# Performance work log

Measured on AMD Instinct MI355X. Metric: run time of the kernel, lower is better.

Reference implementation:

```python
import jax, jax.numpy as jnp
import numpy as np

V, D, NH, HD, FF, NL, NLOOPS = 1056, 320, 5, 64, 864, 6, 8
CAP, EPS, THETA = 0.8, 1e-6, 10000.0
B, S = 8, 2048


def rmsnorm(x, w):
    return w * (x * jax.lax.rsqrt(jnp.mean(x * x, axis=-1, keepdims=True) + EPS))


def rotate_half(x):
    x1, x2 = jnp.split(x, 2, axis=-1)
    return jnp.concatenate([-x2, x1], axis=-1)


def rope_tables(seq_len):
    freqs = 1.0 / (THETA ** (jnp.arange(0, HD, 2, dtype=jnp.float32) / HD))  # [HD/2]
    t = jnp.arange(seq_len, dtype=jnp.float32)
    f = jnp.outer(t, freqs)                      # [S, HD/2]
    f = jnp.concatenate([f, f], axis=-1)         # [S, HD]
    return jnp.cos(f), jnp.sin(f)


def setup_inputs() -> dict:
    key = jax.random.key(0)
    ks = jax.random.split(key, 12)
    std = 0.02
    inp = {
        "input_ids": jax.random.randint(ks[0], (B, S), 0, V),
        "iteration": 0,
        "embedding": jax.random.normal(ks[1], (V, D), jnp.float32),
        "iter_emb": jax.random.normal(ks[2], (NLOOPS, D), jnp.float32),
        "attn_norm_w": jnp.ones((NL, D), jnp.float32),
        "Wqkv": jax.random.normal(ks[3], (NL, 3 * D, D), jnp.float32) * std,
        "wo_w": jax.random.normal(ks[4], (NL, D, D), jnp.float32) * std,
        "router_w": jax.random.normal(ks[5], (NL, D), jnp.float32) * std,
        "mlp_norm_w": jnp.ones((NL, D), jnp.float32),
        "gate_w": jax.random.normal(ks[6], (NL, FF, D), jnp.float32) * std,
        "up_w": jax.random.normal(ks[7], (NL, FF, D), jnp.float32) * std,
        "down_w": jax.random.normal(ks[8], (NL, D, FF), jnp.float32) * std,
        "final_norm_w": jnp.ones((D,), jnp.float32),
    }
    return inp


def reference(input_ids, iteration, embedding, iter_emb, attn_norm_w, Wqkv, wo_w,
              router_w, mlp_norm_w, gate_w, up_w, down_w, final_norm_w):
    batch, seq = input_ids.shape
    k = max(1, int(seq * CAP))
    cos, sin = rope_tables(seq)                 # [S, HD]
    cos4 = cos[None, :, None, :]                # [1,S,1,HD]
    sin4 = sin[None, :, None, :]

    x = embedding[input_ids]                    # [B,S,D]
    if iteration < NLOOPS:
        x = x + iter_emb[iteration][None, None, :]

    causal = jnp.tril(jnp.ones((seq, seq), dtype=bool))
    bidx = jnp.arange(batch)[:, None]           # [B,1]

    for l in range(NL):
        # --- attention block ---
        h = rmsnorm(x, attn_norm_w[l])
        qkv = (h @ Wqkv[l].T).reshape(batch, seq, 3, NH, HD)
        q, kk, v = qkv[:, :, 0], qkv[:, :, 1], qkv[:, :, 2]   # [B,S,H,HD]
        q = q * cos4 + rotate_half(q) * sin4
        kk = kk * cos4 + rotate_half(kk) * sin4
        q, kk, v = (t.transpose(0, 2, 1, 3) for t in (q, kk, v))  # [B,H,S,HD]
        scores = jnp.einsum("bhqd,bhkd->bhqk", q, kk) / np.sqrt(HD)
        scores = jnp.where(causal, scores, -jnp.inf)
        attn = jax.nn.softmax(scores, axis=-1)
        out = jnp.einsum("bhqk,bhkd->bhqd", attn, v)
        out = out.transpose(0, 2, 1, 3).reshape(batch, seq, D)
        x = x + out @ wo_w[l].T

        # --- MoD router + SwiGLU MLP on selected tokens ---
        probs = jax.nn.sigmoid(x @ router_w[l])            # [B,S]
        topk_probs, topk_idx = jax.lax.top_k(probs, k)     # [B,K]
        sel = jnp.take_along_axis(x, topk_idx[:, :, None], axis=1)  # [B,K,D]
        hs = rmsnorm(sel, mlp_norm_w[l])
        gate = jax.nn.silu(hs @ gate_w[l].T) * (hs @ up_w[l].T)
        mlp = (gate @ down_w[l].T) * topk_probs[:, :, None]         # [B,K,D]
        x = x.at[bidx, topk_idx].add(mlp)                  # unique idx: add == scatter-set+residual

    return rmsnorm(x, final_norm_w)
```

## Files before the change

### kernel.cpp

```cpp
#include <hip/hip_runtime.h>
#include <hip/hip_bf16.h>
#include <math.h>

#define VSZ 1056
#define DD 320
#define NH 5
#define HD 64
#define FF 864
#define NL 6
#define NLOOPS 8
#define BB 8
#define SL 2048
#define KK 1638
#define EPSF 1e-6f

typedef _Float16 f16x8 __attribute__((ext_vector_type(8)));
typedef _Float16 f16x4 __attribute__((ext_vector_type(4)));
typedef float floatx16 __attribute__((ext_vector_type(16)));

__device__ inline void gll16(const void* g, void* l) {
    __builtin_amdgcn_global_load_lds((const __attribute__((address_space(1))) void*)g,
                                     (__attribute__((address_space(3))) void*)l, 16, 0, 0);
}

__global__ __launch_bounds__(256) void cast4_kernel(const float* __restrict__ s,
        _Float16* __restrict__ d, int n4) {
    int i = blockIdx.x * 256 + threadIdx.x;
    if (i >= n4) return;
    float4 v = ((const float4*)s)[i];
    f16x4 o = { (_Float16)v.x, (_Float16)v.y, (_Float16)v.z, (_Float16)v.w };
    *(f16x4*)(d + (size_t)i * 4) = o;
}

__global__ __launch_bounds__(256) void embed_kernel(const int* __restrict__ ids,
        const int* __restrict__ iter, const float* __restrict__ emb,
        const float* __restrict__ iter_emb, float* __restrict__ x) {
    int i = blockIdx.x * 256 + threadIdx.x;
    int d = i % DD, bs = i / DD;
    float v = emb[(size_t)ids[bs] * DD + d];
    int it = iter[0];
    if (it < NLOOPS) v += iter_emb[it * DD + d];
    x[i] = v;
}

template<typename OT>
__global__ __launch_bounds__(256) void rmsnorm_kernel(const float* __restrict__ x,
        const float* __restrict__ w, OT* __restrict__ out, int nrows) {
    int row = blockIdx.x * 4 + (threadIdx.x >> 6);
    int lane = threadIdx.x & 63;
    if (row >= nrows) return;
    const float* xr = x + (size_t)row * DD;
    float v[5]; float ss = 0.f;
#pragma unroll
    for (int i = 0; i < 5; ++i) { v[i] = xr[lane + i * 64]; ss += v[i] * v[i]; }
#pragma unroll
    for (int o = 32; o > 0; o >>= 1) ss += __shfl_xor(ss, o);
    float r = rsqrtf(ss * (1.f / DD) + EPSF);
    OT* orow = out + (size_t)row * DD;
#pragma unroll
    for (int i = 0; i < 5; ++i) orow[lane + i * 64] = (OT)(w[lane + i * 64] * v[i] * r);
}

__global__ __launch_bounds__(256) void gather_rmsnorm_kernel(const float* __restrict__ x,
        const int* __restrict__ tkidx, const float* __restrict__ w,
        _Float16* __restrict__ out, int nrows) {
    int row = blockIdx.x * 4 + (threadIdx.x >> 6);
    int lane = threadIdx.x & 63;
    if (row >= nrows) return;
    int b = row / KK;
    int t = tkidx[row];
    const float* xr = x + ((size_t)b * SL + t) * DD;
    float v[5]; float ss = 0.f;
#pragma unroll
    for (int i = 0; i < 5; ++i) { v[i] = xr[lane + i * 64]; ss += v[i] * v[i]; }
#pragma unroll
    for (int o = 32; o > 0; o >>= 1) ss += __shfl_xor(ss, o);
    float r = rsqrtf(ss * (1.f / DD) + EPSF);
    _Float16* orow = out + (size_t)row * DD;
#pragma unroll
    for (int i = 0; i < 5; ++i) orow[lane + i * 64] = (_Float16)(w[lane + i * 64] * v[i] * r);
}

__global__ __launch_bounds__(256) void router_kernel(const float* __restrict__ x,
        const float* __restrict__ rw, float* __restrict__ probs, int nrows) {
    int row = blockIdx.x * 4 + (threadIdx.x >> 6);
    int lane = threadIdx.x & 63;
    if (row >= nrows) return;
    const float* xr = x + (size_t)row * DD;
    float ss = 0.f;
#pragma unroll
    for (int i = 0; i < 5; ++i) ss += xr[lane + i * 64] * rw[lane + i * 64];
#pragma unroll
    for (int o = 32; o > 0; o >>= 1) ss += __shfl_xor(ss, o);
    if (lane == 0) probs[row] = 1.f / (1.f + __expf(-ss));
}

__global__ __launch_bounds__(1024) void topk_kernel(const float* __restrict__ probs,
        int* __restrict__ tkidx, float* __restrict__ tkprob) {
    __shared__ int hist[256];
    __shared__ int scn[256];
    __shared__ int outc;
    __shared__ int s_digit, s_rem;
    int b = blockIdx.x, tid = threadIdx.x;
    unsigned long long k0, k1;
    {
        unsigned int f0 = __float_as_uint(probs[b * SL + tid]);
        unsigned int f1 = __float_as_uint(probs[b * SL + tid + 1024]);
        k0 = ((unsigned long long)f0 << 32) | (unsigned int)(2047 - tid);
        k1 = ((unsigned long long)f1 << 32) | (unsigned int)(2047 - (tid + 1024));
    }
    if (tid == 0) outc = 0;
    unsigned long long prefix = 0, pmask = 0;
    int target = KK;
    for (int shift = 56; shift >= 0; shift -= 8) {
        if (tid < 256) hist[tid] = 0;
        __syncthreads();
        bool a0 = (k0 & pmask) == prefix;
        bool a1 = (k1 & pmask) == prefix;
        int d0 = (int)((k0 >> shift) & 255);
        int d1 = (int)((k1 >> shift) & 255);
        if (a0) atomicAdd(&hist[d0], 1);
        if (a1) atomicAdd(&hist[d1], 1);
        __syncthreads();
        if (tid < 256) scn[tid] = hist[tid];
        __syncthreads();
#pragma unroll
        for (int st = 1; st < 256; st <<= 1) {
            int v = 0;
            if (tid < 256 && tid + st < 256) v = scn[tid + st];
            __syncthreads();
            if (tid < 256) scn[tid] += v;
            __syncthreads();
        }
        if (tid < 256 && hist[tid] > 0) {
            int S = scn[tid];
            int Sgt = S - hist[tid];
            if (Sgt < target && target <= S) { s_digit = tid; s_rem = target - Sgt; }
        }
        __syncthreads();
        int dsel = s_digit, rem = s_rem;
        bool full = (rem == hist[dsel]);
        if (a0 && (d0 > dsel || (full && d0 == dsel))) {
            int s = atomicAdd(&outc, 1);
            tkidx[b * KK + s] = 2047 - (int)(k0 & 0xffffffffu);
            tkprob[b * KK + s] = __uint_as_float((unsigned int)(k0 >> 32));
        }
        if (a1 && (d1 > dsel || (full && d1 == dsel))) {
            int s = atomicAdd(&outc, 1);
            tkidx[b * KK + s] = 2047 - (int)(k1 & 0xffffffffu);
            tkprob[b * KK + s] = __uint_as_float((unsigned int)(k1 >> 32));
        }
        if (full) break;
        target = rem;
        prefix |= ((unsigned long long)dsel) << shift;
        pmask  |= ((unsigned long long)255) << shift;
        __syncthreads();
    }
}

__global__ __launch_bounds__(256) void prep_kernel(const _Float16* __restrict__ qkv,
        _Float16* __restrict__ Qh, _Float16* __restrict__ Kt, _Float16* __restrict__ Vt) {
    __shared__ _Float16 vt[64][72];
    int tid = threadIdx.x;
    int t = blockIdx.x, h = blockIdx.y, b = blockIdx.z;
    int bh = b * NH + h;
    int c = tid >> 5;
    int slb = tid & 31;
    const float QS = 0.125f * 1.44269504088896341f;
#pragma unroll
    for (int half = 0; half < 2; ++half) {
        int sl = half * 32 + slb;
        int s = t * 64 + sl;
        size_t rbase = ((size_t)(b * SL + s) * 3) * (NH * 64) + h * 64;
        f16x8 qv = *(const f16x8*)(qkv + rbase + c * 8);
        f16x8 qp = *(const f16x8*)(qkv + rbase + (c ^ 4) * 8);
        f16x8 kv = *(const f16x8*)(qkv + rbase + NH * 64 + c * 8);
        f16x8 kp = *(const f16x8*)(qkv + rbase + NH * 64 + (c ^ 4) * 8);
        f16x8 vv = *(const f16x8*)(qkv + rbase + 2 * NH * 64 + c * 8);
        f16x8 qo, ko;
#pragma unroll
        for (int j = 0; j < 8; ++j) {
            int d = c * 8 + j;
            float freq = exp2f(-(float)(d & 31) * 0.4152410118609203f);
            float ang = (float)s * freq;
            float cc = cosf(ang), sn = sinf(ang);
            float a = (float)qv[j], p = (float)qp[j];
            float ka = (float)kv[j], kb2 = (float)kp[j];
            float qr = (d < 32) ? a * cc - p * sn : a * cc + p * sn;
            float kr = (d < 32) ? ka * cc - kb2 * sn : ka * cc + kb2 * sn;
            qo[j] = (_Float16)(qr * QS);
            ko[j] = (_Float16)kr;
        }
        *(f16x8*)(Qh + ((size_t)bh * SL + s) * 64 + c * 8) = qo;
        *(f16x8*)(Kt + (((size_t)bh * 32 + t) * 8 + c) * 512 + sl * 8) = ko;
        *(f16x8*)(&vt[sl][c * 8]) = vv;
    }
    __syncthreads();
#pragma unroll
    for (int gg = 0; gg < 2; ++gg) {
        int oo = tid * 16 + gg * 8;
        int kc = oo >> 9;
        int d = (oo >> 3) & 63;
        f16x8 vo;
#pragma unroll
        for (int j = 0; j < 8; ++j) vo[j] = vt[kc * 8 + j][d];
        *(f16x8*)(Vt + (((size_t)bh * 32 + t) * 8 + kc) * 512 + d * 8) = vo;
    }
}

__global__ __launch_bounds__(256, 2) void attn_mfma(const _Float16* __restrict__ Qh,
        const _Float16* __restrict__ Kt, const _Float16* __restrict__ Vt,
        _Float16* __restrict__ attn_out) {
    __shared__ float red[4][64][33];
    __shared__ float msh[4][32];
    __shared__ float lsh[4][32];
    int tid = threadIdx.x;
    int w = tid >> 6;
    int lane = tid & 63;
    int l31 = lane & 31, h5 = lane >> 5;
    int g = blockIdx.x;
    int j = g >> 3;
    int bh = (g & 7) + 8 * (j >> 6);
    int qt = 63 - (j & 63);
    int b = bh / NH, h = bh % NH;
    int nt = (qt >> 1) + 1;
    int qw = qt * 32;
    int myq = qw + l31;

    f16x8 qf[4];
    const _Float16* qrow = Qh + ((size_t)bh * SL + myq) * 64;
#pragma unroll
    for (int kd = 0; kd < 4; ++kd) qf[kd] = *(const f16x8*)(qrow + kd * 16 + h5 * 8);

    const _Float16* Kb = Kt + (size_t)bh * 32 * 4096;
    const _Float16* Vb = Vt + (size_t)bh * 32 * 4096;

    floatx16 O0, O1;
#pragma unroll
    for (int r = 0; r < 16; ++r) { O0[r] = 0.f; O1[r] = 0.f; }
    float m = -INFINITY, l = 0.f;

    for (int t = w; t < nt; t += 4) {
        const _Float16* kb = Kb + (size_t)t * 4096;
        const _Float16* vb = Vb + (size_t)t * 4096;
        f16x8 a0[4], a1[4], v0[4], v1[4];
#pragma unroll
        for (int kd = 0; kd < 4; ++kd) {
            int off = (kd * 2 + h5) * 512 + l31 * 8;
            a0[kd] = *(const f16x8*)(kb + off);
            a1[kd] = *(const f16x8*)(kb + off + 256);
        }
#pragma unroll
        for (int kc = 0; kc < 4; ++kc) {
            int off = (kc * 2 + h5) * 512 + l31 * 8;
            v0[kc] = *(const f16x8*)(vb + off);
            v1[kc] = *(const f16x8*)(vb + off + 256);
        }
        floatx16 S0, S1;
#pragma unroll
        for (int r = 0; r < 16; ++r) { S0[r] = 0.f; S1[r] = 0.f; }
#pragma unroll
        for (int kd = 0; kd < 4; ++kd) {
            S0 = __builtin_amdgcn_mfma_f32_32x32x16_f16(a0[kd], qf[kd], S0, 0, 0, 0);
            S1 = __builtin_amdgcn_mfma_f32_32x32x16_f16(a1[kd], qf[kd], S1, 0, 0, 0);
        }
        int t0 = t * 64;
        if (t0 + 63 > qw) {
#pragma unroll
            for (int r = 0; r < 16; ++r) {
                int key = t0 + (r & 3) + 8 * (r >> 2) + 4 * h5;
                if (key > myq) S0[r] = -INFINITY;
                if (key + 32 > myq) S1[r] = -INFINITY;
            }
        }
        float tmax = S0[0];
#pragma unroll
        for (int r = 1; r < 16; ++r) tmax = fmaxf(tmax, S0[r]);
#pragma unroll
        for (int r = 0; r < 16; ++r) tmax = fmaxf(tmax, S1[r]);
        tmax = fmaxf(tmax, __shfl_xor(tmax, 32));
        if (__any(tmax > m + 8.f)) {
            float mnew = fmaxf(m, tmax);
            float alpha = exp2f(m - mnew);
            l *= alpha; O0 *= alpha; O1 *= alpha; m = mnew;
        }
        float P0[16], P1[16]; float psum = 0.f;
#pragma unroll
        for (int r = 0; r < 16; ++r) { P0[r] = exp2f(S0[r] - m); psum += P0[r]; }
#pragma unroll
        for (int r = 0; r < 16; ++r) { P1[r] = exp2f(S1[r] - m); psum += P1[r]; }
        psum += __shfl_xor(psum, 32);
        l += psum;
#pragma unroll
        for (int sub = 0; sub < 2; ++sub) {
            const float* P = sub ? P1 : P0;
#pragma unroll
            for (int kk = 0; kk < 2; ++kk) {
                float lo[4], hi[4], plo[4], phi[4];
#pragma unroll
                for (int k = 0; k < 4; ++k) { lo[k] = P[kk * 8 + k]; hi[k] = P[kk * 8 + 4 + k]; }
#pragma unroll
                for (int k = 0; k < 4; ++k) { plo[k] = __shfl_xor(lo[k], 32); phi[k] = __shfl_xor(hi[k], 32); }
                f16x8 pf;
#pragma unroll
                for (int k = 0; k < 4; ++k) {
                    pf[k]     = (_Float16)(h5 ? phi[k] : lo[k]);
                    pf[4 + k] = (_Float16)(h5 ? hi[k] : plo[k]);
                }
                int ksg = sub * 2 + kk;
                O0 = __builtin_amdgcn_mfma_f32_32x32x16_f16(v0[ksg], pf, O0, 0, 0, 0);
                O1 = __builtin_amdgcn_mfma_f32_32x32x16_f16(v1[ksg], pf, O1, 0, 0, 0);
            }
        }
    }
    if (h5 == 0) msh[w][l31] = m;
    __syncthreads();
    float M = fmaxf(fmaxf(msh[0][l31], msh[1][l31]), fmaxf(msh[2][l31], msh[3][l31]));
    float wgt = exp2f(m - M);
    if (h5 == 0) lsh[w][l31] = l * wgt;
#pragma unroll
    for (int r = 0; r < 16; ++r) {
        int d = (r & 3) + 8 * (r >> 2) + 4 * h5;
        red[w][d][l31] = O0[r] * wgt;
        red[w][d + 32][l31] = O1[r] * wgt;
    }
    __syncthreads();
    float lsum = lsh[0][l31] + lsh[1][l31] + lsh[2][l31] + lsh[3][l31];
    float linv = 1.f / lsum;
    f16x8 ov;
#pragma unroll
    for (int k = 0; k < 8; ++k) {
        int d = w * 16 + h5 * 8 + k;
        ov[k] = (_Float16)((red[0][d][l31] + red[1][d][l31] +
                            red[2][d][l31] + red[3][d][l31]) * linv);
    }
    *(f16x8*)(attn_out + ((size_t)(b * SL + myq)) * DD + h * 64 + w * 16 + h5 * 8) = ov;
}

template<int MODE>
__global__ __launch_bounds__(256) void gemm_mfma(const _Float16* __restrict__ A,
        const _Float16* __restrict__ W, _Float16* __restrict__ Ch, float* __restrict__ X,
        int M, int N, int K, const int* __restrict__ sidx, const float* __restrict__ sprob) {
    __shared__ __attribute__((aligned(16))) _Float16 As[4096];
    __shared__ __attribute__((aligned(16))) _Float16 Ws[4096];
    int tid = threadIdx.x;
    int lane = tid & 63;
    int wave = tid >> 6;
    int l31 = lane & 31, h5 = lane >> 5;
    int m0 = blockIdx.y * 128, n0 = blockIdx.x * 128;
    int wm = (wave & 1) * 64, wn = (wave >> 1) * 64;

    int srow = tid & 127;
    int skc = tid >> 7;
    int arow = m0 + srow; if (arow >= M) arow = M - 1;
    int wrow = n0 + srow; if (wrow >= N) wrow = N - 1;
    const _Float16* Ag = A + (size_t)arow * K + skc * 8;
    const _Float16* Wg = W + (size_t)wrow * K + skc * 8;
    _Float16* AsD = As + (size_t)(tid & ~63) * 8;
    _Float16* WsD = Ws + (size_t)(tid & ~63) * 8;

    floatx16 acc[2][2];
#pragma unroll
    for (int i = 0; i < 2; ++i)
#pragma unroll
        for (int j = 0; j < 2; ++j)
#pragma unroll
            for (int r = 0; r < 16; ++r) acc[i][j][r] = 0.f;

    for (int k0 = 0; k0 < K; k0 += 32) {
        __syncthreads();
        gll16(Ag + k0, AsD);
        gll16(Ag + k0 + 16, AsD + 2048);
        gll16(Wg + k0, WsD);
        gll16(Wg + k0 + 16, WsD + 2048);
        __syncthreads();
#pragma unroll
        for (int ks = 0; ks < 2; ++ks) {
            int kc = ks * 2 + h5;
            f16x8 a0 = *(const f16x8*)(As + kc * 1024 + (wm + l31) * 8);
            f16x8 a1 = *(const f16x8*)(As + kc * 1024 + (wm + 32 + l31) * 8);
            f16x8 b0 = *(const f16x8*)(Ws + kc * 1024 + (wn + l31) * 8);
            f16x8 b1 = *(const f16x8*)(Ws + kc * 1024 + (wn + 32 + l31) * 8);
            acc[0][0] = __builtin_amdgcn_mfma_f32_32x32x16_f16(a0, b0, acc[0][0], 0, 0, 0);
            acc[0][1] = __builtin_amdgcn_mfma_f32_32x32x16_f16(a0, b1, acc[0][1], 0, 0, 0);
            acc[1][0] = __builtin_amdgcn_mfma_f32_32x32x16_f16(a1, b0, acc[1][0], 0, 0, 0);
            acc[1][1] = __builtin_amdgcn_mfma_f32_32x32x16_f16(a1, b1, acc[1][1], 0, 0, 0);
        }
    }

#pragma unroll
    for (int ti = 0; ti < 2; ++ti) {
#pragma unroll
        for (int r = 0; r < 16; ++r) {
            int mm = m0 + wm + ti * 32 + (r & 3) + 8 * (r >> 2) + 4 * h5;
            if (mm >= M) continue;
            float scale = 1.f;
            float* xrow = nullptr;
            _Float16* crow = nullptr;
            if (MODE == 2) {
                int b = mm / KK;
                scale = sprob[mm];
                xrow = X + ((size_t)(b * SL + sidx[mm])) * N;
            } else if (MODE == 1) {
                xrow = X + (size_t)mm * N;
            } else {
                crow = Ch + (size_t)mm * N;
            }
#pragma unroll
            for (int tj = 0; tj < 2; ++tj) {
                int nn = n0 + wn + tj * 32 + l31;
                if (nn >= N) continue;
                float v = acc[ti][tj][r];
                if (MODE == 0) crow[nn] = (_Float16)v;
                else if (MODE == 1) xrow[nn] += v;
                else xrow[nn] += v * scale;
            }
        }
    }
}

__global__ __launch_bounds__(256) void gemm_gateup(const _Float16* __restrict__ A,
        const _Float16* __restrict__ Wg, const _Float16* __restrict__ Wu,
        _Float16* __restrict__ Ch, int M, int N, int K) {
    __shared__ __attribute__((aligned(16))) _Float16 As[4096];
    __shared__ __attribute__((aligned(16))) _Float16 Wgs[4096];
    __shared__ __attribute__((aligned(16))) _Float16 Wus[4096];
    int tid = threadIdx.x;
    int lane = tid & 63;
    int wave = tid >> 6;
    int l31 = lane & 31, h5 = lane >> 5;
    int m0 = blockIdx.y * 128, n0 = blockIdx.x * 128;
    int wm = (wave & 1) * 64, wn = (wave >> 1) * 64;

    int srow = tid & 127;
    int skc = tid >> 7;
    int arow = m0 + srow; if (arow >= M) arow = M - 1;
    int wrow = n0 + srow; if (wrow >= N) wrow = N - 1;
    const _Float16* Ag  = A  + (size_t)arow * K + skc * 8;
    const _Float16* Wgg = Wg + (size_t)wrow * K + skc * 8;
    const _Float16* Wug = Wu + (size_t)wrow * K + skc * 8;
    _Float16* AsD  = As  + (size_t)(tid & ~63) * 8;
    _Float16* WgsD = Wgs + (size_t)(tid & ~63) * 8;
    _Float16* WusD = Wus + (size_t)(tid & ~63) * 8;

    floatx16 ag[2][2], au[2][2];
#pragma unroll
    for (int i = 0; i < 2; ++i)
#pragma unroll
        for (int j = 0; j < 2; ++j)
#pragma unroll
            for (int r = 0; r < 16; ++r) { ag[i][j][r] = 0.f; au[i][j][r] = 0.f; }

    for (int k0 = 0; k0 < K; k0 += 32) {
        __syncthreads();
        gll16(Ag + k0, AsD);
        gll16(Ag + k0 + 16, AsD + 2048);
        gll16(Wgg + k0, WgsD);
        gll16(Wgg + k0 + 16, WgsD + 2048);
        gll16(Wug + k0, WusD);
        gll16(Wug + k0 + 16, WusD + 2048);
        __syncthreads();
#pragma unroll
        for (int ks = 0; ks < 2; ++ks) {
            int kc = ks * 2 + h5;
            f16x8 a0 = *(const f16x8*)(As + kc * 1024 + (wm + l31) * 8);
            f16x8 a1 = *(const f16x8*)(As + kc * 1024 + (wm + 32 + l31) * 8);
            f16x8 g0 = *(const f16x8*)(Wgs + kc * 1024 + (wn + l31) * 8);
            f16x8 g1f = *(const f16x8*)(Wgs + kc * 1024 + (wn + 32 + l31) * 8);
            f16x8 u0 = *(const f16x8*)(Wus + kc * 1024 + (wn + l31) * 8);
            f16x8 u1 = *(const f16x8*)(Wus + kc * 1024 + (wn + 32 + l31) * 8);
            ag[0][0] = __builtin_amdgcn_mfma_f32_32x32x16_f16(a0, g0, ag[0][0], 0, 0, 0);
            ag[0][1] = __builtin_amdgcn_mfma_f32_32x32x16_f16(a0, g1f, ag[0][1], 0, 0, 0);
            ag[1][0] = __builtin_amdgcn_mfma_f32_32x32x16_f16(a1, g0, ag[1][0], 0, 0, 0);
            ag[1][1] = __builtin_amdgcn_mfma_f32_32x32x16_f16(a1, g1f, ag[1][1], 0, 0, 0);
            au[0][0] = __builtin_amdgcn_mfma_f32_32x32x16_f16(a0, u0, au[0][0], 0, 0, 0);
            au[0][1] = __builtin_amdgcn_mfma_f32_32x32x16_f16(a0, u1, au[0][1], 0, 0, 0);
            au[1][0] = __builtin_amdgcn_mfma_f32_32x32x16_f16(a1, u0, au[1][0], 0, 0, 0);
            au[1][1] = __builtin_amdgcn_mfma_f32_32x32x16_f16(a1, u1, au[1][1], 0, 0, 0);
        }
    }

#pragma unroll
    for (int ti = 0; ti < 2; ++ti) {
#pragma unroll
        for (int r = 0; r < 16; ++r) {
            int mm = m0 + wm + ti * 32 + (r & 3) + 8 * (r >> 2) + 4 * h5;
            if (mm >= M) continue;
            _Float16* crow = Ch + (size_t)mm * N;
#pragma unroll
            for (int tj = 0; tj < 2; ++tj) {
                int nn = n0 + wn + tj * 32 + l31;
                if (nn >= N) continue;
                float gv = ag[ti][tj][r], uv = au[ti][tj][r];
                crow[nn] = (_Float16)((gv / (1.f + __expf(-gv))) * uv);
            }
        }
    }
}

extern "C" void kernel_launch(void* const* d_in, const int* in_sizes, int n_in,
                              void* d_out, int out_size, void* d_ws, size_t ws_size,
                              hipStream_t stream) {
    const int*   ids          = (const int*)d_in[0];
    const int*   iter         = (const int*)d_in[1];
    const float* emb          = (const float*)d_in[2];
    const float* iter_emb     = (const float*)d_in[3];
    const float* attn_norm_w  = (const float*)d_in[4];
    const float* Wqkv         = (const float*)d_in[5];
    const float* wo_w         = (const float*)d_in[6];
    const float* router_w     = (const float*)d_in[7];
    const float* mlp_norm_w   = (const float*)d_in[8];
    const float* gate_w       = (const float*)d_in[9];
    const float* up_w         = (const float*)d_in[10];
    const float* down_w       = (const float*)d_in[11];
    const float* final_norm_w = (const float*)d_in[12];
    float* out = (float*)d_out;

    const size_t XN   = (size_t)BB * SL * DD;
    const size_t QKVN = (size_t)BB * SL * 3 * DD;
    const size_t HN   = (size_t)BB * NH * SL * 64;
    char* ws = (char*)d_ws;
    size_t off = 0;
    float*    x        = (float*)(ws + off);    off += XN * 4;
    _Float16* h        = (_Float16*)(ws + off); off += XN * 2;
    _Float16* attn_out = (_Float16*)(ws + off); off += XN * 2;
    float*    probs    = (float*)(ws + off);    off += (size_t)BB * SL * 4;
    int*      tkidx    = (int*)(ws + off);      off += (size_t)BB * KK * 4;
    float*    tkprob   = (float*)(ws + off);    off += (size_t)BB * KK * 4;
    off = (off + 255) & ~(size_t)255;
    _Float16* qkvh     = (_Float16*)(ws + off); off += QKVN * 2;
    _Float16* Qh       = (_Float16*)(ws + off); off += HN * 2;
    _Float16* Kh       = (_Float16*)(ws + off); off += HN * 2;
    _Float16* Vh       = (_Float16*)(ws + off); off += HN * 2;
    _Float16* WqkvH    = (_Float16*)(ws + off);
    _Float16* woH   = WqkvH + (size_t)NL * 3 * DD * DD;
    _Float16* gateH = woH   + (size_t)NL * DD * DD;
    _Float16* upH   = gateH + (size_t)NL * FF * DD;
    _Float16* downH = upH   + (size_t)NL * FF * DD;
    _Float16* g1 = qkvh;

    cast4_kernel<<<(NL * 3 * DD * DD / 4 + 255) / 256, 256, 0, stream>>>(Wqkv, WqkvH, NL * 3 * DD * DD / 4);
    cast4_kernel<<<(NL * DD * DD / 4 + 255) / 256, 256, 0, stream>>>(wo_w, woH, NL * DD * DD / 4);
    cast4_kernel<<<(NL * FF * DD / 4 + 255) / 256, 256, 0, stream>>>(gate_w, gateH, NL * FF * DD / 4);
    cast4_kernel<<<(NL * FF * DD / 4 + 255) / 256, 256, 0, stream>>>(up_w, upH, NL * FF * DD / 4);
    cast4_kernel<<<(NL * DD * FF / 4 + 255) / 256, 256, 0, stream>>>(down_w, downH, NL * DD * FF / 4);

    embed_kernel<<<20480, 256, 0, stream>>>(ids, iter, emb, iter_emb, x);

    const int M1 = BB * SL;
    const int M2 = BB * KK;
    for (int l = 0; l < NL; ++l) {
        rmsnorm_kernel<_Float16><<<4096, 256, 0, stream>>>(x, attn_norm_w + l * DD, h, M1);
        gemm_mfma<0><<<dim3(8, 128), 256, 0, stream>>>(h, WqkvH + (size_t)l * 3 * DD * DD,
                                                       qkvh, nullptr, M1, 3 * DD, DD, nullptr, nullptr);
        prep_kernel<<<dim3(SL / 64, NH, BB), 256, 0, stream>>>(qkvh, Qh, Kh, Vh);
        attn_mfma<<<BB * NH * (SL / 32), 256, 0, stream>>>(Qh, Kh, Vh, attn_out);
        gemm_mfma<1><<<dim3(3, 128), 256, 0, stream>>>(attn_out, woH + (size_t)l * DD * DD,
                                                       nullptr, x, M1, DD, DD, nullptr, nullptr);
        router_kernel<<<4096, 256, 0, stream>>>(x, router_w + l * DD, probs, M1);
        topk_kernel<<<BB, 1024, 0, stream>>>(probs, tkidx, tkprob);
        gather_rmsnorm_kernel<<<3276, 256, 0, stream>>>(x, tkidx, mlp_norm_w + l * DD, h, M2);
        gemm_gateup<<<dim3(7, 103), 256, 0, stream>>>(h, gateH + (size_t)l * FF * DD,
                                                      upH + (size_t)l * FF * DD, g1, M2, FF, DD);
        gemm_mfma<2><<<dim3(3, 103), 256, 0, stream>>>(g1, downH + (size_t)l * DD * FF,
                                                       nullptr, x, M2, DD, FF, tkidx, tkprob);
    }
    rmsnorm_kernel<float><<<4096, 256, 0, stream>>>(x, final_norm_w, out, M1);
}
```

Measured before the change: 1.809 ms.

## Split-K residual GEMMs with atomics and remove P shuffles in attention

The wo and down-projection GEMMs now split K across blockIdx.z (2 and 4 ways) and accumulate into the residual with unsafeAtomicAdd. This raises block counts for these small-N GEMMs, which previously launched few blocks. Attention drops the cross-lane shuffles that rearranged P before the PV MFMA: the V transpose in prep is permuted to match the MFMA output layout, and P is packed with cvt_pkrtz. The reduction LDS buffer is halved by writing O0 and O1 in two passes. The risks are atomic contention, nondeterministic summation order, and round-toward-zero conversion of P.

Measured after the change: 1.966 ms. 1.09x slower.

```diff
diff --git a/kernel.cpp b/kernel.cpp
--- a/kernel.cpp
+++ b/kernel.cpp
@@ -203,7 +203,10 @@
         int d = (oo >> 3) & 63;
         f16x8 vo;
 #pragma unroll
-        for (int j = 0; j < 8; ++j) vo[j] = vt[kc * 8 + j][d];
+        for (int j = 0; j < 8; ++j) {
+            int key = (kc >> 1) * 16 + (j & 3) + 8 * (j >> 2) + 4 * (kc & 1);
+            vo[j] = vt[key][d];
+        }
         *(f16x8*)(Vt + (((size_t)bh * 32 + t) * 8 + kc) * 512 + d * 8) = vo;
     }
 }
@@ -211,7 +214,7 @@
 __global__ __launch_bounds__(256, 2) void attn_mfma(const _Float16* __restrict__ Qh,
         const _Float16* __restrict__ Kt, const _Float16* __restrict__ Vt,
         _Float16* __restrict__ attn_out) {
-    __shared__ float red[4][64][33];
+    __shared__ float red[4][32][32];
     __shared__ float msh[4][32];
     __shared__ float lsh[4][32];
     int tid = threadIdx.x;
@@ -295,19 +298,17 @@
         for (int sub = 0; sub < 2; ++sub) {
             const float* P = sub ? P1 : P0;
 #pragma unroll
-            for (int kk = 0; kk < 2; ++kk) {
-                float lo[4], hi[4], plo[4], phi[4];
-#pragma unroll
-                for (int k = 0; k < 4; ++k) { lo[k] = P[kk * 8 + k]; hi[k] = P[kk * 8 + 4 + k]; }
-#pragma unroll
-                for (int k = 0; k < 4; ++k) { plo[k] = __shfl_xor(lo[k], 32); phi[k] = __shfl_xor(hi[k], 32); }
+            for (int kc = 0; kc < 2; ++kc) {
+                auto q01 = __builtin_amdgcn_cvt_pkrtz(P[kc * 8 + 0], P[kc * 8 + 1]);
+                auto q23 = __builtin_amdgcn_cvt_pkrtz(P[kc * 8 + 2], P[kc * 8 + 3]);
+                auto q45 = __builtin_amdgcn_cvt_pkrtz(P[kc * 8 + 4], P[kc * 8 + 5]);
+                auto q67 = __builtin_amdgcn_cvt_pkrtz(P[kc * 8 + 6], P[kc * 8 + 7]);
                 f16x8 pf;
-#pragma unroll
-                for (int k = 0; k < 4; ++k) {
-                    pf[k]     = (_Float16)(h5 ? phi[k] : lo[k]);
-                    pf[4 + k] = (_Float16)(h5 ? hi[k] : plo[k]);
-                }
-                int ksg = sub * 2 + kk;
+                pf[0] = (_Float16)q01[0]; pf[1] = (_Float16)q01[1];
+                pf[2] = (_Float16)q23[0]; pf[3] = (_Float16)q23[1];
+                pf[4] = (_Float16)q45[0]; pf[5] = (_Float16)q45[1];
+                pf[6] = (_Float16)q67[0]; pf[7] = (_Float16)q67[1];
+                int ksg = sub * 2 + kc;
                 O0 = __builtin_amdgcn_mfma_f32_32x32x16_f16(v0[ksg], pf, O0, 0, 0, 0);
                 O1 = __builtin_amdgcn_mfma_f32_32x32x16_f16(v1[ksg], pf, O1, 0, 0, 0);
             }
@@ -322,25 +323,43 @@
     for (int r = 0; r < 16; ++r) {
         int d = (r & 3) + 8 * (r >> 2) + 4 * h5;
         red[w][d][l31] = O0[r] * wgt;
-        red[w][d + 32][l31] = O1[r] * wgt;
     }
     __syncthreads();
     float lsum = lsh[0][l31] + lsh[1][l31] + lsh[2][l31] + lsh[3][l31];
     float linv = 1.f / lsum;
-    f16x8 ov;
-#pragma unroll
-    for (int k = 0; k < 8; ++k) {
-        int d = w * 16 + h5 * 8 + k;
-        ov[k] = (_Float16)((red[0][d][l31] + red[1][d][l31] +
-                            red[2][d][l31] + red[3][d][l31]) * linv);
-    }
-    *(f16x8*)(attn_out + ((size_t)(b * SL + myq)) * DD + h * 64 + w * 16 + h5 * 8) = ov;
+    if (w < 2) {
+        f16x8 ov;
+#pragma unroll
+        for (int k = 0; k < 8; ++k) {
+            int d = w * 16 + h5 * 8 + k;
+            ov[k] = (_Float16)((red[0][d][l31] + red[1][d][l31] +
+                                red[2][d][l31] + red[3][d][l31]) * linv);
+        }
+        *(f16x8*)(attn_out + ((size_t)(b * SL + myq)) * DD + h * 64 + w * 16 + h5 * 8) = ov;
+    }
+    __syncthreads();
+#pragma unroll
+    for (int r = 0; r < 16; ++r) {
+        int d = (r & 3) + 8 * (r >> 2) + 4 * h5;
+        red[w][d][l31] = O1[r] * wgt;
+    }
+    __syncthreads();
+    if (w >= 2) {
+        f16x8 ov;
+#pragma unroll
+        for (int k = 0; k < 8; ++k) {
+            int d = (w - 2) * 16 + h5 * 8 + k;
+            ov[k] = (_Float16)((red[0][d][l31] + red[1][d][l31] +
+                                red[2][d][l31] + red[3][d][l31]) * linv);
+        }
+        *(f16x8*)(attn_out + ((size_t)(b * SL + myq)) * DD + h * 64 + 32 + (w - 2) * 16 + h5 * 8) = ov;
+    }
 }
 
 template<int MODE>
 __global__ __launch_bounds__(256) void gemm_mfma(const _Float16* __restrict__ A,
         const _Float16* __restrict__ W, _Float16* __restrict__ Ch, float* __restrict__ X,
-        int M, int N, int K, const int* __restrict__ sidx, const float* __restrict__ sprob) {
+        int M, int N, int K, int klen, const int* __restrict__ sidx, const float* __restrict__ sprob) {
     __shared__ __attribute__((aligned(16))) _Float16 As[4096];
     __shared__ __attribute__((aligned(16))) _Float16 Ws[4096];
     int tid = threadIdx.x;
@@ -349,6 +368,8 @@
     int l31 = lane & 31, h5 = lane >> 5;
     int m0 = blockIdx.y * 128, n0 = blockIdx.x * 128;
     int wm = (wave & 1) * 64, wn = (wave >> 1) * 64;
+    int kbeg = blockIdx.z * klen;
+    int kend = kbeg + klen; if (kend > K) kend = K;
 
     int srow = tid & 127;
     int skc = tid >> 7;
@@ -367,7 +388,7 @@
 #pragma unroll
             for (int r = 0; r < 16; ++r) acc[i][j][r] = 0.f;
 
-    for (int k0 = 0; k0 < K; k0 += 32) {
+    for (int k0 = kbeg; k0 < kend; k0 += 32) {
         __syncthreads();
         gll16(Ag + k0, AsD);
         gll16(Ag + k0 + 16, AsD + 2048);
@@ -412,8 +433,8 @@
                 if (nn >= N) continue;
                 float v = acc[ti][tj][r];
                 if (MODE == 0) crow[nn] = (_Float16)v;
-                else if (MODE == 1) xrow[nn] += v;
-                else xrow[nn] += v * scale;
+                else if (MODE == 1) unsafeAtomicAdd(&xrow[nn], v);
+                else unsafeAtomicAdd(&xrow[nn], v * scale);
             }
         }
     }
@@ -551,19 +572,19 @@
     const int M2 = BB * KK;
     for (int l = 0; l < NL; ++l) {
         rmsnorm_kernel<_Float16><<<4096, 256, 0, stream>>>(x, attn_norm_w + l * DD, h, M1);
-        gemm_mfma<0><<<dim3(8, 128), 256, 0, stream>>>(h, WqkvH + (size_t)l * 3 * DD * DD,
-                                                       qkvh, nullptr, M1, 3 * DD, DD, nullptr, nullptr);
+        gemm_mfma<0><<<dim3(8, 128, 1), 256, 0, stream>>>(h, WqkvH + (size_t)l * 3 * DD * DD,
+                                                       qkvh, nullptr, M1, 3 * DD, DD, DD, nullptr, nullptr);
         prep_kernel<<<dim3(SL / 64, NH, BB), 256, 0, stream>>>(qkvh, Qh, Kh, Vh);
         attn_mfma<<<BB * NH * (SL / 32), 256, 0, stream>>>(Qh, Kh, Vh, attn_out);
-        gemm_mfma<1><<<dim3(3, 128), 256, 0, stream>>>(attn_out, woH + (size_t)l * DD * DD,
-                                                       nullptr, x, M1, DD, DD, nullptr, nullptr);
+        gemm_mfma<1><<<dim3(3, 128, 2), 256, 0, stream>>>(attn_out, woH + (size_t)l * DD * DD,
+                                                       nullptr, x, M1, DD, DD, 160, nullptr, nullptr);
         router_kernel<<<4096, 256, 0, stream>>>(x, router_w + l * DD, probs, M1);
         topk_kernel<<<BB, 1024, 0, stream>>>(probs, tkidx, tkprob);
         gather_rmsnorm_kernel<<<3276, 256, 0, stream>>>(x, tkidx, mlp_norm_w + l * DD, h, M2);
         gemm_gateup<<<dim3(7, 103), 256, 0, stream>>>(h, gateH + (size_t)l * FF * DD,
                                                       upH + (size_t)l * FF * DD, g1, M2, FF, DD);
-        gemm_mfma<2><<<dim3(3, 103), 256, 0, stream>>>(g1, downH + (size_t)l * DD * FF,
-                                                       nullptr, x, M2, DD, FF, tkidx, tkprob);
+        gemm_mfma<2><<<dim3(3, 103, 4), 256, 0, stream>>>(g1, downH + (size_t)l * DD * FF,
+                                                       nullptr, x, M2, DD, FF, 224, tkidx, tkprob);
     }
     rmsnorm_kernel<float><<<4096, 256, 0, stream>>>(x, final_norm_w, out, M1);
 }
```
